# Kernel optimization log

Measured on AMD Instinct MI355X. Metric: run time of the kernel, lower is better.

## Reference

```python
import jax, jax.numpy as jnp
import numpy as np

WS = 4           # window size (cubic)
NUM_HEADS = 4
DIM = 128
NW = 392         # number of windows per sample
B = 8            # batch
N = WS ** 3      # 64 tokens per window


def _relative_position_index(ws):
    coords = np.stack(np.meshgrid(np.arange(ws), np.arange(ws), np.arange(ws), indexing='ij'))  # [3,ws,ws,ws]
    flat = coords.reshape(3, -1)                      # [3, ws^3]
    rel = flat[:, :, None] - flat[:, None, :]         # [3, N, N]
    rel = rel.transpose(1, 2, 0).copy()               # [N, N, 3]
    rel += ws - 1
    rel[:, :, 0] *= (2 * ws - 1) ** 2
    rel[:, :, 1] *= (2 * ws - 1)
    return rel.sum(-1)                                # [N, N] int


def setup_inputs() -> dict:
    key = jax.random.key(0)
    ks = jax.random.split(key, 8)
    B_ = NW * B
    x = jax.random.normal(ks[0], (B_, N, DIM), dtype=jnp.float32)
    mask = jax.random.normal(ks[1], (NW, N, N), dtype=jnp.float32)
    # learned params
    qkv_w = jax.random.normal(ks[2], (3 * DIM, DIM), dtype=jnp.float32) * 0.02
    qkv_b = jnp.zeros((3 * DIM,), dtype=jnp.float32)
    proj_w = jax.random.normal(ks[3], (DIM, DIM), dtype=jnp.float32) * 0.02
    proj_b = jnp.zeros((DIM,), dtype=jnp.float32)
    tbl = jax.random.normal(ks[4], ((2 * WS - 1) ** 3, NUM_HEADS), dtype=jnp.float32) * 0.02
    rel_index = jnp.asarray(_relative_position_index(WS), dtype=jnp.int32)  # [N, N]
    return {"x": x, "mask": mask, "qkv_w": qkv_w, "qkv_b": qkv_b,
            "proj_w": proj_w, "proj_b": proj_b, "rpb_table": tbl,
            "rel_index": rel_index}


def reference(x, mask, qkv_w, qkv_b, proj_w, proj_b, rpb_table, rel_index):
    B_, N_, C = x.shape
    H = NUM_HEADS
    hd = C // H
    scale = hd ** (-0.5)
    # qkv projection: [B_, N, 3, H, hd] -> (3, B_, H, N, hd)
    qkv = (x @ qkv_w.T + qkv_b).reshape(B_, N_, 3, H, hd).transpose(2, 0, 3, 1, 4)
    q, k, v = qkv[0], qkv[1], qkv[2]
    attn = jnp.einsum('bhnd,bhmd->bhnm', q * scale, k)        # [B_, H, N, N]
    # gathered relative position bias: [N, N, H] -> [H, N, N]
    rpe = rpb_table[rel_index].transpose(2, 0, 1)
    attn = attn + rpe[None]
    nW = mask.shape[0]
    attn = attn.reshape(B_ // nW, nW, H, N_, N_) + mask[None, :, None]
    attn = attn.reshape(B_, H, N_, N_)
    attn = jax.nn.softmax(attn, axis=-1)
    out = jnp.einsum('bhnm,bhmd->bnhd', attn, v).reshape(B_, N_, C)
    return out @ proj_w.T + proj_b
```

## Files before the change

### kernel.cpp

```cpp
#include <hip/hip_runtime.h>
#include <hip/hip_bf16.h>


typedef __bf16 bf16x8 __attribute__((ext_vector_type(8)));
typedef __bf16 bf16x4 __attribute__((ext_vector_type(4)));
typedef float f32x4 __attribute__((ext_vector_type(4)));

#define NWMASK 392
#define SCALE 0.17677669529663687f

__global__ void prep(const float* __restrict__ qkv_w, const float* __restrict__ proj_w,
                     const float* __restrict__ tbl, const int* __restrict__ ridx,
                     __bf16* __restrict__ wqkv, __bf16* __restrict__ wproj,
                     float* __restrict__ rpe_t,
                     const float* __restrict__ mask, float* __restrict__ mask_t,
                     int do_mask) {
    __shared__ float t[64][65];
    if (blockIdx.x < 320) {
        int i = blockIdx.x * 256 + threadIdx.x;
        if (i < 49152) {
            wqkv[i] = (__bf16)qkv_w[i];
        } else if (i < 65536) {
            int j = i - 49152;  wproj[j] = (__bf16)proj_w[j];
        } else {
            int j = i - 65536;
            rpe_t[j] = tbl[ridx[(j & 63) * 64 + ((j >> 6) & 63)] * 4 + (j >> 12)];
        }
    } else {
        if (!do_mask) return;
        const int w = blockIdx.x - 320;
        const int c = threadIdx.x & 63, rb = threadIdx.x >> 6;
        const float* src = mask + (size_t)w * 4096;
        #pragma unroll
        for (int i = 0; i < 16; ++i) { int r = rb * 16 + i; t[r][c] = src[r * 64 + c]; }
        __syncthreads();
        float* dst = mask_t + (size_t)w * 4096;
        #pragma unroll
        for (int i = 0; i < 16; ++i) { int r = rb * 16 + i; dst[r * 64 + c] = t[c][r]; }
    }
}

template<bool TB>
__global__ __launch_bounds__(256, 4) void wattn_main(
    const float* __restrict__ x, const float* __restrict__ maskp,
    const float* __restrict__ qkv_b, const float* __restrict__ proj_b,
    const __bf16* __restrict__ wqkv, const __bf16* __restrict__ wproj,
    const float* __restrict__ rpe_t, float* __restrict__ out)
{
    __shared__ __align__(16) __bf16 smem[13824];
    const int win  = blockIdx.x;
    const int tid  = threadIdx.x;
    const int h    = tid >> 6;
    const int lane = tid & 63;
    const int quad = lane >> 4;
    const int l16  = lane & 15;

    __bf16* const xs  = smem;
    __bf16* const buf = smem + 8704 + h * 1280;

    {
        const float* xb = x + (size_t)win * 8192;
        #pragma unroll
        for (int i = 0; i < 2; ++i) {
            const int row  = h * 16 + (lane >> 3) + i * 8;
            const int colg = (lane & 7) * 16;
            const float* xp = xb + row * 128 + colg;
            float4 a0 = *(const float4*)(xp);
            float4 a1 = *(const float4*)(xp + 4);
            float4 a2 = *(const float4*)(xp + 8);
            float4 a3 = *(const float4*)(xp + 12);
            bf16x8 t0, t1;
            t0[0]=(__bf16)a0.x; t0[1]=(__bf16)a0.y; t0[2]=(__bf16)a0.z; t0[3]=(__bf16)a0.w;
            t0[4]=(__bf16)a1.x; t0[5]=(__bf16)a1.y; t0[6]=(__bf16)a1.z; t0[7]=(__bf16)a1.w;
            t1[0]=(__bf16)a2.x; t1[1]=(__bf16)a2.y; t1[2]=(__bf16)a2.z; t1[3]=(__bf16)a2.w;
            t1[4]=(__bf16)a3.x; t1[5]=(__bf16)a3.y; t1[6]=(__bf16)a3.z; t1[7]=(__bf16)a3.w;
            *(bf16x8*)(xs + row * 136 + colg)     = t0;
            *(bf16x8*)(xs + row * 136 + colg + 8) = t1;
        }
    }

    bf16x8 kwf[2][4]; f32x4 kb4[2];
    #pragma unroll
    for (int nt = 0; nt < 2; ++nt) {
        const int ng = 128 + h * 32 + nt * 16 + l16;
        kb4[nt] = *(const f32x4*)(qkv_b + 128 + h * 32 + nt * 16 + quad * 4);
        #pragma unroll
        for (int kt = 0; kt < 4; ++kt)
            kwf[nt][kt] = *(const bf16x8*)(wqkv + ng * 128 + kt * 32 + quad * 8);
    }
    __syncthreads();

    bf16x8 kf[4], qf[4], vf[2][2];

    #pragma unroll
    for (int half = 0; half < 2; ++half) {
        #pragma unroll
        for (int m2 = 0; m2 < 2; ++m2) {
            const int mt = half * 2 + m2;
            bf16x8 af[4];
            #pragma unroll
            for (int kt = 0; kt < 4; ++kt)
                af[kt] = *(const bf16x8*)(xs + (mt * 16 + l16) * 136 + kt * 32 + quad * 8);
            #pragma unroll
            for (int nt = 0; nt < 2; ++nt) {
                f32x4 acc = {0.f, 0.f, 0.f, 0.f};
                #pragma unroll
                for (int kt = 0; kt < 4; ++kt)
                    acc = __builtin_amdgcn_mfma_f32_16x16x32_bf16(kwf[nt][kt], af[kt], acc, 0, 0, 0);
                bf16x4 pk;
                #pragma unroll
                for (int r = 0; r < 4; ++r) pk[r] = (__bf16)(acc[r] + kb4[nt][r]);
                *(bf16x4*)(buf + (m2 * 16 + l16) * 40 + nt * 16 + quad * 4) = pk;
            }
        }
        kf[half * 2 + 0] = *(const bf16x8*)(buf + l16 * 40 + quad * 8);
        kf[half * 2 + 1] = *(const bf16x8*)(buf + (16 + l16) * 40 + quad * 8);
    }

    {
        bf16x8 qwf[2][4]; f32x4 qb4[2];
        #pragma unroll
        for (int nt = 0; nt < 2; ++nt) {
            const int ng = h * 32 + nt * 16 + l16;
            qb4[nt] = *(const f32x4*)(qkv_b + h * 32 + nt * 16 + quad * 4);
            #pragma unroll
            for (int kt = 0; kt < 4; ++kt)
                qwf[nt][kt] = *(const bf16x8*)(wqkv + ng * 128 + kt * 32 + quad * 8);
        }
        #pragma unroll
        for (int half = 0; half < 2; ++half) {
            #pragma unroll
            for (int m2 = 0; m2 < 2; ++m2) {
                const int mt = half * 2 + m2;
                bf16x8 af[4];
                #pragma unroll
                for (int kt = 0; kt < 4; ++kt)
                    af[kt] = *(const bf16x8*)(xs + (mt * 16 + l16) * 136 + kt * 32 + quad * 8);
                #pragma unroll
                for (int nt = 0; nt < 2; ++nt) {
                    f32x4 acc = {0.f, 0.f, 0.f, 0.f};
                    #pragma unroll
                    for (int kt = 0; kt < 4; ++kt)
                        acc = __builtin_amdgcn_mfma_f32_16x16x32_bf16(qwf[nt][kt], af[kt], acc, 0, 0, 0);
                    bf16x4 pk;
                    #pragma unroll
                    for (int r = 0; r < 4; ++r) pk[r] = (__bf16)((acc[r] + qb4[nt][r]) * SCALE);
                    *(bf16x4*)(buf + (m2 * 16 + l16) * 40 + nt * 16 + quad * 4) = pk;
                }
            }
            qf[half * 2 + 0] = *(const bf16x8*)(buf + l16 * 40 + quad * 8);
            qf[half * 2 + 1] = *(const bf16x8*)(buf + (16 + l16) * 40 + quad * 8);
        }
    }

    {
        bf16x8 vwf[2][4]; float vbb[2];
        #pragma unroll
        for (int nt = 0; nt < 2; ++nt) {
            const int ng = 256 + h * 32 + nt * 16 + l16;
            vbb[nt] = qkv_b[ng];
            #pragma unroll
            for (int kt = 0; kt < 4; ++kt)
                vwf[nt][kt] = *(const bf16x8*)(wqkv + ng * 128 + kt * 32 + quad * 8);
        }
        #pragma unroll
        for (int half = 0; half < 2; ++half) {
            #pragma unroll
            for (int m2 = 0; m2 < 2; ++m2) {
                const int mt = half * 2 + m2;
                bf16x8 af[4];
                #pragma unroll
                for (int kt = 0; kt < 4; ++kt)
                    af[kt] = *(const bf16x8*)(xs + (mt * 16 + l16) * 136 + kt * 32 + quad * 8);
                #pragma unroll
                for (int nt = 0; nt < 2; ++nt) {
                    f32x4 acc = {0.f, 0.f, 0.f, 0.f};
                    #pragma unroll
                    for (int kt = 0; kt < 4; ++kt)
                        acc = __builtin_amdgcn_mfma_f32_16x16x32_bf16(af[kt], vwf[nt][kt], acc, 0, 0, 0);
                    bf16x4 pk;
                    #pragma unroll
                    for (int r = 0; r < 4; ++r) pk[r] = (__bf16)(acc[r] + vbb[nt]);
                    *(bf16x4*)(buf + (nt * 16 + l16) * 40 + m2 * 16 + quad * 4) = pk;
                }
            }
            #pragma unroll
            for (int nf = 0; nf < 2; ++nf)
                vf[half][nf] = *(const bf16x8*)(buf + (nf * 16 + l16) * 40 + quad * 8);
        }
    }

    const int wm = win % NWMASK;
    const float* rt = rpe_t + h * 4096;
    const float* mw = maskp + (size_t)wm * 4096;
    f32x4 rb4[4], mb4[4];
    #pragma unroll
    for (int nt = 0; nt < 4; ++nt) {
        rb4[nt] = *(const f32x4*)(rt + (nt * 16 + l16) * 64 + quad * 4);
        if constexpr (TB)
            mb4[nt] = *(const f32x4*)(mw + (nt * 16 + l16) * 64 + quad * 4);
    }
    __syncthreads();

    bf16x8 onesf;
    #pragma unroll
    for (int j = 0; j < 8; ++j) onesf[j] = (__bf16)1.0f;

    #pragma unroll
    for (int mt = 0; mt < 4; ++mt) {
        f32x4 sc[4];
        #pragma unroll
        for (int nt = 0; nt < 4; ++nt) {
            f32x4 z = {0.f, 0.f, 0.f, 0.f};
            sc[nt] = __builtin_amdgcn_mfma_f32_16x16x32_bf16(qf[mt], kf[nt], z, 0, 0, 0);
        }
        float mbs[4][4];
        if constexpr (!TB) {
            #pragma unroll
            for (int nt = 0; nt < 4; ++nt)
                #pragma unroll
                for (int r = 0; r < 4; ++r)
                    mbs[nt][r] = mw[(mt * 16 + quad * 4 + r) * 64 + nt * 16 + l16];
        }
        #pragma unroll
        for (int nt = 0; nt < 4; ++nt)
            #pragma unroll
            for (int r = 0; r < 4; ++r) {
                const float m = TB ? mb4[nt][r] : mbs[nt][r];
                buf[(quad * 4 + r) * 72 + nt * 16 + l16] =
                    (__bf16)__expf(sc[nt][r] + rb4[nt][r] + m);
            }
        if (mt < 3) {
            #pragma unroll
            for (int nt = 0; nt < 4; ++nt) {
                rb4[nt] = *(const f32x4*)(rt + (nt * 16 + l16) * 64 + (mt + 1) * 16 + quad * 4);
                if constexpr (TB)
                    mb4[nt] = *(const f32x4*)(mw + (nt * 16 + l16) * 64 + (mt + 1) * 16 + quad * 4);
            }
        }
        f32x4 oa[2] = {{0.f,0.f,0.f,0.f},{0.f,0.f,0.f,0.f}};
        f32x4 os = {0.f, 0.f, 0.f, 0.f};
        #pragma unroll
        for (int kt = 0; kt < 2; ++kt) {
            bf16x8 pf = *(const bf16x8*)(buf + l16 * 72 + kt * 32 + quad * 8);
            oa[0] = __builtin_amdgcn_mfma_f32_16x16x32_bf16(pf, vf[kt][0], oa[0], 0, 0, 0);
            oa[1] = __builtin_amdgcn_mfma_f32_16x16x32_bf16(pf, vf[kt][1], oa[1], 0, 0, 0);
            os    = __builtin_amdgcn_mfma_f32_16x16x32_bf16(pf, onesf,     os,    0, 0, 0);
        }
        #pragma unroll
        for (int r = 0; r < 4; ++r) {
            const float inv = 1.0f / os[r];
            const int orow = mt * 16 + quad * 4 + r;
            xs[orow * 136 + h * 32 + l16]      = (__bf16)(oa[0][r] * inv);
            xs[orow * 136 + h * 32 + 16 + l16] = (__bf16)(oa[1][r] * inv);
        }
    }
    __syncthreads();

    bf16x8 of[4];
    #pragma unroll
    for (int kt = 0; kt < 4; ++kt)
        of[kt] = *(const bf16x8*)(xs + (h * 16 + l16) * 136 + kt * 32 + quad * 8);
    #pragma unroll
    for (int nt = 0; nt < 8; ++nt) {
        const int ng = nt * 16 + l16;
        const float b = proj_b[ng];
        bf16x8 wf[4];
        #pragma unroll
        for (int kt = 0; kt < 4; ++kt)
            wf[kt] = *(const bf16x8*)(wproj + ng * 128 + kt * 32 + quad * 8);
        f32x4 acc = {0.f, 0.f, 0.f, 0.f};
        #pragma unroll
        for (int kt = 0; kt < 4; ++kt)
            acc = __builtin_amdgcn_mfma_f32_16x16x32_bf16(of[kt], wf[kt], acc, 0, 0, 0);
        float* dst = out + ((size_t)win * 64 + h * 16 + quad * 4) * 128 + ng;
        #pragma unroll
        for (int r = 0; r < 4; ++r) dst[(size_t)r * 128] = acc[r] + b;
    }
}

extern "C" void kernel_launch(void* const* d_in, const int* in_sizes, int n_in,
                              void* d_out, int out_size, void* d_ws, size_t ws_size,
                              hipStream_t stream) {
    const float* x      = (const float*)d_in[0];
    const float* mask   = (const float*)d_in[1];
    const float* qkv_w  = (const float*)d_in[2];
    const float* qkv_b  = (const float*)d_in[3];
    const float* proj_w = (const float*)d_in[4];
    const float* proj_b = (const float*)d_in[5];
    const float* tbl    = (const float*)d_in[6];
    const int*   ridx   = (const int*)d_in[7];
    float* out = (float*)d_out;

    __bf16* wqkv  = (__bf16*)d_ws;
    __bf16* wproj = wqkv + 384 * 128;
    float*  rpe_t = (float*)((char*)d_ws + 131072);
    float*  mask_t = (float*)((char*)d_ws + 196608);
    const size_t need_tb = 196608 + (size_t)NWMASK * 4096 * 4;
    const bool tb = ws_size >= need_tb;

    prep<<<tb ? 712 : 320, 256, 0, stream>>>(qkv_w, proj_w, tbl, ridx,
                                             wqkv, wproj, rpe_t, mask, mask_t,
                                             tb ? 1 : 0);
    if (tb)
        wattn_main<true><<<3136, 256, 0, stream>>>(x, mask_t, qkv_b, proj_b,
                                                   wqkv, wproj, rpe_t, out);
    else
        wattn_main<false><<<3136, 256, 0, stream>>>(x, mask, qkv_b, proj_b,
                                                    wqkv, wproj, rpe_t, out);
}
```

Before: 301.8 us.

## Hoist Q weights, single-pass QKV staging, double-buffer P, prefetch proj weights

Loads the Q and K weight fragments together up front. The K/Q/V projections now run over all 64 rows in one pass through an enlarged per-head LDS buffer instead of two halves, and the MFMA operand order is swapped so results are stored with scalar stores. The softmax probability tile is double-buffered across row tiles to avoid write-after-read stalls. Projection weights and bias are prefetched before the barrier and software-pipelined two tiles ahead. The aim is to hide global-load latency and cut LDS round trips, at the cost of more registers and LDS, which may reduce occupancy.

```diff
diff --git a/kernel.cpp b/kernel.cpp
--- a/kernel.cpp
+++ b/kernel.cpp
@@ -47,7 +47,7 @@
     const __bf16* __restrict__ wqkv, const __bf16* __restrict__ wproj,
     const float* __restrict__ rpe_t, float* __restrict__ out)
 {
-    __shared__ __align__(16) __bf16 smem[13824];
+    __shared__ __align__(16) __bf16 smem[18944];
     const int win  = blockIdx.x;
     const int tid  = threadIdx.x;
     const int h    = tid >> 6;
@@ -56,7 +56,7 @@
     const int l16  = lane & 15;
 
     __bf16* const xs  = smem;
-    __bf16* const buf = smem + 8704 + h * 1280;
+    __bf16* const buf = smem + 8704 + h * 2560;
 
     {
         const float* xb = x + (size_t)win * 8192;
@@ -79,24 +79,27 @@
         }
     }
 
-    bf16x8 kwf[2][4]; f32x4 kb4[2];
+    bf16x8 kwf[2][4]; float kbb[2];
+    bf16x8 qwf[2][4]; float qbb[2];
     #pragma unroll
     for (int nt = 0; nt < 2; ++nt) {
-        const int ng = 128 + h * 32 + nt * 16 + l16;
-        kb4[nt] = *(const f32x4*)(qkv_b + 128 + h * 32 + nt * 16 + quad * 4);
-        #pragma unroll
-        for (int kt = 0; kt < 4; ++kt)
-            kwf[nt][kt] = *(const bf16x8*)(wqkv + ng * 128 + kt * 32 + quad * 8);
+        const int ngk = 128 + h * 32 + nt * 16 + l16;
+        const int ngq = h * 32 + nt * 16 + l16;
+        kbb[nt] = qkv_b[ngk];
+        qbb[nt] = qkv_b[ngq];
+        #pragma unroll
+        for (int kt = 0; kt < 4; ++kt) {
+            kwf[nt][kt] = *(const bf16x8*)(wqkv + ngk * 128 + kt * 32 + quad * 8);
+            qwf[nt][kt] = *(const bf16x8*)(wqkv + ngq * 128 + kt * 32 + quad * 8);
+        }
     }
     __syncthreads();
 
     bf16x8 kf[4], qf[4], vf[2][2];
 
-    #pragma unroll
-    for (int half = 0; half < 2; ++half) {
-        #pragma unroll
-        for (int m2 = 0; m2 < 2; ++m2) {
-            const int mt = half * 2 + m2;
+    {
+        #pragma unroll
+        for (int mt = 0; mt < 4; ++mt) {
             bf16x8 af[4];
             #pragma unroll
             for (int kt = 0; kt < 4; ++kt)
@@ -106,93 +109,77 @@
                 f32x4 acc = {0.f, 0.f, 0.f, 0.f};
                 #pragma unroll
                 for (int kt = 0; kt < 4; ++kt)
-                    acc = __builtin_amdgcn_mfma_f32_16x16x32_bf16(kwf[nt][kt], af[kt], acc, 0, 0, 0);
-                bf16x4 pk;
-                #pragma unroll
-                for (int r = 0; r < 4; ++r) pk[r] = (__bf16)(acc[r] + kb4[nt][r]);
-                *(bf16x4*)(buf + (m2 * 16 + l16) * 40 + nt * 16 + quad * 4) = pk;
-            }
-        }
-        kf[half * 2 + 0] = *(const bf16x8*)(buf + l16 * 40 + quad * 8);
-        kf[half * 2 + 1] = *(const bf16x8*)(buf + (16 + l16) * 40 + quad * 8);
+                    acc = __builtin_amdgcn_mfma_f32_16x16x32_bf16(af[kt], kwf[nt][kt], acc, 0, 0, 0);
+                #pragma unroll
+                for (int r = 0; r < 4; ++r)
+                    buf[(mt * 16 + quad * 4 + r) * 40 + nt * 16 + l16] = (__bf16)(acc[r] + kbb[nt]);
+            }
+        }
+        #pragma unroll
+        for (int j = 0; j < 4; ++j)
+            kf[j] = *(const bf16x8*)(buf + (j * 16 + l16) * 40 + quad * 8);
     }
 
     {
-        bf16x8 qwf[2][4]; f32x4 qb4[2];
-        #pragma unroll
-        for (int nt = 0; nt < 2; ++nt) {
-            const int ng = h * 32 + nt * 16 + l16;
-            qb4[nt] = *(const f32x4*)(qkv_b + h * 32 + nt * 16 + quad * 4);
-            #pragma unroll
-            for (int kt = 0; kt < 4; ++kt)
-                qwf[nt][kt] = *(const bf16x8*)(wqkv + ng * 128 + kt * 32 + quad * 8);
-        }
-        #pragma unroll
-        for (int half = 0; half < 2; ++half) {
-            #pragma unroll
-            for (int m2 = 0; m2 < 2; ++m2) {
-                const int mt = half * 2 + m2;
-                bf16x8 af[4];
+        #pragma unroll
+        for (int mt = 0; mt < 4; ++mt) {
+            bf16x8 af[4];
+            #pragma unroll
+            for (int kt = 0; kt < 4; ++kt)
+                af[kt] = *(const bf16x8*)(xs + (mt * 16 + l16) * 136 + kt * 32 + quad * 8);
+            #pragma unroll
+            for (int nt = 0; nt < 2; ++nt) {
+                f32x4 acc = {0.f, 0.f, 0.f, 0.f};
                 #pragma unroll
                 for (int kt = 0; kt < 4; ++kt)
-                    af[kt] = *(const bf16x8*)(xs + (mt * 16 + l16) * 136 + kt * 32 + quad * 8);
-                #pragma unroll
-                for (int nt = 0; nt < 2; ++nt) {
-                    f32x4 acc = {0.f, 0.f, 0.f, 0.f};
-                    #pragma unroll
-                    for (int kt = 0; kt < 4; ++kt)
-                        acc = __builtin_amdgcn_mfma_f32_16x16x32_bf16(qwf[nt][kt], af[kt], acc, 0, 0, 0);
-                    bf16x4 pk;
-                    #pragma unroll
-                    for (int r = 0; r < 4; ++r) pk[r] = (__bf16)((acc[r] + qb4[nt][r]) * SCALE);
-                    *(bf16x4*)(buf + (m2 * 16 + l16) * 40 + nt * 16 + quad * 4) = pk;
-                }
-            }
-            qf[half * 2 + 0] = *(const bf16x8*)(buf + l16 * 40 + quad * 8);
-            qf[half * 2 + 1] = *(const bf16x8*)(buf + (16 + l16) * 40 + quad * 8);
-        }
+                    acc = __builtin_amdgcn_mfma_f32_16x16x32_bf16(af[kt], qwf[nt][kt], acc, 0, 0, 0);
+                #pragma unroll
+                for (int r = 0; r < 4; ++r)
+                    buf[(mt * 16 + quad * 4 + r) * 40 + nt * 16 + l16] = (__bf16)((acc[r] + qbb[nt]) * SCALE);
+            }
+        }
+        #pragma unroll
+        for (int mt = 0; mt < 4; ++mt)
+            qf[mt] = *(const bf16x8*)(buf + (mt * 16 + l16) * 40 + quad * 8);
     }
 
     {
-        bf16x8 vwf[2][4]; float vbb[2];
+        bf16x8 wf[2][4]; float bb[2];
         #pragma unroll
         for (int nt = 0; nt < 2; ++nt) {
             const int ng = 256 + h * 32 + nt * 16 + l16;
-            vbb[nt] = qkv_b[ng];
-            #pragma unroll
-            for (int kt = 0; kt < 4; ++kt)
-                vwf[nt][kt] = *(const bf16x8*)(wqkv + ng * 128 + kt * 32 + quad * 8);
-        }
-        #pragma unroll
-        for (int half = 0; half < 2; ++half) {
-            #pragma unroll
-            for (int m2 = 0; m2 < 2; ++m2) {
-                const int mt = half * 2 + m2;
-                bf16x8 af[4];
+            bb[nt] = qkv_b[ng];
+            #pragma unroll
+            for (int kt = 0; kt < 4; ++kt)
+                wf[nt][kt] = *(const bf16x8*)(wqkv + ng * 128 + kt * 32 + quad * 8);
+        }
+        #pragma unroll
+        for (int mt = 0; mt < 4; ++mt) {
+            bf16x8 af[4];
+            #pragma unroll
+            for (int kt = 0; kt < 4; ++kt)
+                af[kt] = *(const bf16x8*)(xs + (mt * 16 + l16) * 136 + kt * 32 + quad * 8);
+            #pragma unroll
+            for (int nt = 0; nt < 2; ++nt) {
+                f32x4 acc = {0.f, 0.f, 0.f, 0.f};
                 #pragma unroll
                 for (int kt = 0; kt < 4; ++kt)
-                    af[kt] = *(const bf16x8*)(xs + (mt * 16 + l16) * 136 + kt * 32 + quad * 8);
-                #pragma unroll
-                for (int nt = 0; nt < 2; ++nt) {
-                    f32x4 acc = {0.f, 0.f, 0.f, 0.f};
-                    #pragma unroll
-                    for (int kt = 0; kt < 4; ++kt)
-                        acc = __builtin_amdgcn_mfma_f32_16x16x32_bf16(af[kt], vwf[nt][kt], acc, 0, 0, 0);
-                    bf16x4 pk;
-                    #pragma unroll
-                    for (int r = 0; r < 4; ++r) pk[r] = (__bf16)(acc[r] + vbb[nt]);
-                    *(bf16x4*)(buf + (nt * 16 + l16) * 40 + m2 * 16 + quad * 4) = pk;
-                }
-            }
+                    acc = __builtin_amdgcn_mfma_f32_16x16x32_bf16(af[kt], wf[nt][kt], acc, 0, 0, 0);
+                bf16x4 pk;
+                #pragma unroll
+                for (int r = 0; r < 4; ++r) pk[r] = (__bf16)(acc[r] + bb[nt]);
+                *(bf16x4*)(buf + (nt * 16 + l16) * 72 + mt * 16 + quad * 4) = pk;
+            }
+        }
+        #pragma unroll
+        for (int kt = 0; kt < 2; ++kt)
             #pragma unroll
             for (int nf = 0; nf < 2; ++nf)
-                vf[half][nf] = *(const bf16x8*)(buf + (nf * 16 + l16) * 40 + quad * 8);
-        }
-    }
-
-    const int wm = win % NWMASK;
+                vf[kt][nf] = *(const bf16x8*)(buf + (nf * 16 + l16) * 72 + kt * 32 + quad * 8);
+    }
+
     const float* rt = rpe_t + h * 4096;
-    const float* mw = maskp + (size_t)wm * 4096;
+    const float* mw = maskp + (size_t)(win % NWMASK) * 4096;
     f32x4 rb4[4], mb4[4];
     #pragma unroll
     for (int nt = 0; nt < 4; ++nt) {
@@ -208,6 +195,7 @@
 
     #pragma unroll
     for (int mt = 0; mt < 4; ++mt) {
+        __bf16* const pb = buf + (mt & 1) * 1280;
         f32x4 sc[4];
         #pragma unroll
         for (int nt = 0; nt < 4; ++nt) {
@@ -227,7 +215,7 @@
             #pragma unroll
             for (int r = 0; r < 4; ++r) {
                 const float m = TB ? mb4[nt][r] : mbs[nt][r];
-                buf[(quad * 4 + r) * 72 + nt * 16 + l16] =
+                pb[(quad * 4 + r) * 72 + nt * 16 + l16] =
                     (__bf16)__expf(sc[nt][r] + rb4[nt][r] + m);
             }
         if (mt < 3) {
@@ -242,7 +230,7 @@
         f32x4 os = {0.f, 0.f, 0.f, 0.f};
         #pragma unroll
         for (int kt = 0; kt < 2; ++kt) {
-            bf16x8 pf = *(const bf16x8*)(buf + l16 * 72 + kt * 32 + quad * 8);
+            bf16x8 pf = *(const bf16x8*)(pb + l16 * 72 + kt * 32 + quad * 8);
             oa[0] = __builtin_amdgcn_mfma_f32_16x16x32_bf16(pf, vf[kt][0], oa[0], 0, 0, 0);
             oa[1] = __builtin_amdgcn_mfma_f32_16x16x32_bf16(pf, vf[kt][1], oa[1], 0, 0, 0);
             os    = __builtin_amdgcn_mfma_f32_16x16x32_bf16(pf, onesf,     os,    0, 0, 0);
@@ -255,6 +243,16 @@
             xs[orow * 136 + h * 32 + 16 + l16] = (__bf16)(oa[1][r] * inv);
         }
     }
+
+    float pbv[8];
+    #pragma unroll
+    for (int nt = 0; nt < 8; ++nt) pbv[nt] = proj_b[nt * 16 + l16];
+    bf16x8 wfp[2][4];
+    #pragma unroll
+    for (int t = 0; t < 2; ++t)
+        #pragma unroll
+        for (int kt = 0; kt < 4; ++kt)
+            wfp[t][kt] = *(const bf16x8*)(wproj + (t * 16 + l16) * 128 + kt * 32 + quad * 8);
     __syncthreads();
 
     bf16x8 of[4];
@@ -263,19 +261,18 @@
         of[kt] = *(const bf16x8*)(xs + (h * 16 + l16) * 136 + kt * 32 + quad * 8);
     #pragma unroll
     for (int nt = 0; nt < 8; ++nt) {
-        const int ng = nt * 16 + l16;
-        const float b = proj_b[ng];
-        bf16x8 wf[4];
+        f32x4 acc = {0.f, 0.f, 0.f, 0.f};
         #pragma unroll
         for (int kt = 0; kt < 4; ++kt)
-            wf[kt] = *(const bf16x8*)(wproj + ng * 128 + kt * 32 + quad * 8);
-        f32x4 acc = {0.f, 0.f, 0.f, 0.f};
-        #pragma unroll
-        for (int kt = 0; kt < 4; ++kt)
-            acc = __builtin_amdgcn_mfma_f32_16x16x32_bf16(of[kt], wf[kt], acc, 0, 0, 0);
-        float* dst = out + ((size_t)win * 64 + h * 16 + quad * 4) * 128 + ng;
-        #pragma unroll
-        for (int r = 0; r < 4; ++r) dst[(size_t)r * 128] = acc[r] + b;
+            acc = __builtin_amdgcn_mfma_f32_16x16x32_bf16(of[kt], wfp[nt & 1][kt], acc, 0, 0, 0);
+        if (nt < 6) {
+            #pragma unroll
+            for (int kt = 0; kt < 4; ++kt)
+                wfp[nt & 1][kt] = *(const bf16x8*)(wproj + ((nt + 2) * 16 + l16) * 128 + kt * 32 + quad * 8);
+        }
+        float* dst = out + ((size_t)win * 64 + h * 16 + quad * 4) * 128 + nt * 16 + l16;
+        #pragma unroll
+        for (int r = 0; r < 4; ++r) dst[(size_t)r * 128] = acc[r] + pbv[nt];
     }
 }
 
```

Result: slower. 314.9 us (+4.4%).
